# Optimization experiments

Measured on AMD Instinct MI355X. Metric: run time of the kernel, lower is better.

Reference implementation:

```python
import jax, jax.numpy as jnp
import numpy as np
import math

D_MODEL, N_HEADS, D_FF = 512, 8, 2048
B, S = 4, 2048
EPS = 1e-6


def _layernorm(x, alpha, bias):
    # Faithful to the torch module: std is unbiased (ddof=1) and eps is added to std, not var.
    m = jnp.mean(x, axis=-1, keepdims=True)
    s = jnp.std(x, axis=-1, keepdims=True, ddof=1)
    return alpha * (x - m) / (s + EPS) + bias


def setup_inputs() -> dict:
    key = jax.random.key(0)
    ks = jax.random.split(key, 16)
    d, f = D_MODEL, D_FF
    sd = 1.0 / math.sqrt(d)
    sf = 1.0 / math.sqrt(f)
    return {
        "x": jax.random.normal(ks[0], (B, S, d), jnp.float32),
        "wq": jax.random.normal(ks[1], (d, d), jnp.float32) * sd,
        "bq": jnp.zeros((d,), jnp.float32),
        "wk": jax.random.normal(ks[2], (d, d), jnp.float32) * sd,
        "bk": jnp.zeros((d,), jnp.float32),
        "wv": jax.random.normal(ks[3], (d, d), jnp.float32) * sd,
        "bv": jnp.zeros((d,), jnp.float32),
        "wo": jax.random.normal(ks[4], (d, d), jnp.float32) * sd,
        "bo": jnp.zeros((d,), jnp.float32),
        "w1": jax.random.normal(ks[5], (d, f), jnp.float32) * sd,
        "b1": jnp.zeros((f,), jnp.float32),
        "w2": jax.random.normal(ks[6], (f, d), jnp.float32) * sf,
        "b2": jnp.zeros((d,), jnp.float32),
        "ln1_a": jnp.ones((d,), jnp.float32),
        "ln1_b": jnp.zeros((d,), jnp.float32),
        "ln2_a": jnp.ones((d,), jnp.float32),
        "ln2_b": jnp.zeros((d,), jnp.float32),
    }


def reference(x, wq, bq, wk, bk, wv, bv, wo, bo, w1, b1, w2, b2, ln1_a, ln1_b, ln2_a, ln2_b):
    b, s, d = x.shape
    h, dk = N_HEADS, d // N_HEADS
    # QKV projections -> [b, h, s, dk]
    q = (x @ wq + bq).reshape(b, s, h, dk).transpose(0, 2, 1, 3)
    k = (x @ wk + bk).reshape(b, s, h, dk).transpose(0, 2, 1, 3)
    v = (x @ wv + bv).reshape(b, s, h, dk).transpose(0, 2, 1, 3)
    # Manual scaled-dot-product attention (no mask in EncoderBlock path)
    scores = jnp.einsum("bhqd,bhkd->bhqk", q, k) / jnp.sqrt(jnp.float32(dk))
    probs = jax.nn.softmax(scores, axis=-1)
    attn = jnp.einsum("bhqk,bhkd->bhqd", probs, v)
    concat = attn.transpose(0, 2, 1, 3).reshape(b, s, d)
    mha_out = concat @ wo + bo
    # Residual + LayerNorm 1
    y = _layernorm(x + mha_out, ln1_a, ln1_b)
    # FFN + Residual + LayerNorm 2
    ff = jax.nn.relu(y @ w1 + b1) @ w2 + b2
    return _layernorm(y + ff, ln2_a, ln2_b)
```

## Files before the change

### kernel.cpp

```cpp
#include <hip/hip_runtime.h>
#include <hip/hip_bf16.h>


typedef __bf16 bf16;
typedef __bf16 bf16x4 __attribute__((ext_vector_type(4)));
typedef __bf16 bf16x8 __attribute__((ext_vector_type(8)));
typedef float  f32x4  __attribute__((ext_vector_type(4)));

#define NBATCH 4
#define SEQ    2048
#define DMODEL 512
#define NHEADS 8
#define DHEAD  64
#define DFF    2048
#define MTOT   (NBATCH * SEQ)
#define WS_NEED 73416704u
#define QSCALE (0.125f * 1.44269504f)

__device__ __forceinline__ f32x4 mfma16(bf16x8 a, bf16x8 b, f32x4 c) {
    return __builtin_amdgcn_mfma_f32_16x16x32_bf16(a, b, c, 0, 0, 0);
}

__device__ __forceinline__ void lds16(const bf16* g, bf16* l) {
    __builtin_amdgcn_global_load_lds(
        (const __attribute__((address_space(1))) void*)g,
        (__attribute__((address_space(3))) void*)l, 16, 0, 0);
}

__device__ __forceinline__ float scrub(float f) {
    return (fabsf(f) < 1e30f) ? f : 0.f;
}

__device__ __forceinline__ void xcd_swizzle(int BMv, int BNv, int& mb, int& nb) {
    int gx = gridDim.x, gy = gridDim.y;
    int lin = blockIdx.y * gx + blockIdx.x;
    int q = (gx * gy) >> 3;
    lin = (lin & 7) * q + (lin >> 3);
    int mbi = lin / gy, nbi = lin - mbi * gy;
    mb = mbi * BMv; nb = nbi * BNv;
}

__global__ void sentinel_kernel(bf16* out) {
    out[threadIdx.x] = (bf16)1000.0f;
}

__global__ __launch_bounds__(256) void prep_kernel(
        const float* x,
        const float* wq, const float* wk, const float* wv, const float* wo,
        const float* w1, const float* w2,
        const float* bq, const float* bk, const float* bv, const float* bo,
        const float* b1, const float* b2,
        const float* l1a, const float* l1b, const float* l2a, const float* l2b,
        bf16* __restrict__ xcv,
        bf16* __restrict__ wT, bf16* __restrict__ w1T, bf16* __restrict__ w2T,
        bf16* __restrict__ prm) {
    __shared__ bf16 tile[32][33];
    int b = blockIdx.x;
    if (b < 4096) {
        int i = (b * 256 + threadIdx.x) * 4;
        float4 f = *(const float4*)(x + i);
        bf16x4 o = {(bf16)scrub(f.x), (bf16)scrub(f.y),
                    (bf16)scrub(f.z), (bf16)scrub(f.w)};
        *(bf16x4*)(xcv + i) = o;
        return;
    }
    if (b < 4106) {
        int pb = b - 4096;
        const float* srcs[10] = {bq, bk, bv, bo, b1, b2, l1a, l1b, l2a, l2b};
        const int len[10] = {512,512,512,512,2048,512,512,512,512,512};
        const int dst[10] = {0,512,1024,1536,2048,4096,4608,5120,5632,6144};
        const float* s = srcs[pb];
        bf16* d = prm + dst[pb];
        for (int i = threadIdx.x; i < len[pb]; i += 256)
            d[i] = (bf16)scrub(s[i]);
        return;
    }
    const float* in; bf16* out; int K, N, bx, by;
    if (b < 5130) {
        int idx = b - 4106, z = idx >> 8, rem = idx & 255;
        const float* srcs[4] = {wq, wk, wv, wo};
        in = srcs[z]; out = wT + (size_t)z * 262144;
        K = 512; N = 512; bx = rem & 15; by = rem >> 4;
    } else if (b < 6154) {
        int idx = b - 5130;
        in = w1; out = w1T; K = 512; N = 2048; bx = idx & 63; by = idx >> 6;
    } else {
        int idx = b - 6154;
        in = w2; out = w2T; K = 2048; N = 512; bx = idx & 15; by = idx >> 4;
    }
    int tx = threadIdx.x & 31, ty = threadIdx.x >> 5;
    int n0 = bx * 32, k0 = by * 32;
#pragma unroll
    for (int i = 0; i < 4; i++) {
        int kl = ty * 4 + i;
        tile[kl][tx] = (bf16)scrub(in[(size_t)(k0 + kl) * N + n0 + tx]);
    }
    __syncthreads();
#pragma unroll
    for (int i = 0; i < 4; i++) {
        int nl = ty * 4 + i;
        out[(size_t)(n0 + nl) * K + k0 + tx] = tile[tx][nl];
    }
}

template <bool RELU>
__global__ __launch_bounds__(256) void gemm_bt(
        const bf16* __restrict__ A, const bf16* __restrict__ BT,
        const bf16* __restrict__ bias, bf16* __restrict__ Cout,
        int M, int N, int K) {
    constexpr int BM = 128, BN = 128;
    __shared__ __align__(16) bf16 As0[BM * 32], As1[BM * 32];
    __shared__ __align__(16) bf16 Bs0[BN * 32], Bs1[BN * 32];

    int tid  = threadIdx.x;
    int wid  = tid >> 6, lane = tid & 63;
    int quad = lane >> 4, l15 = lane & 15;
    int mb, nb;
    xcd_swizzle(BM, BN, mb, nb);
    int wm = (wid >> 1) * 64, wn = (wid & 1) * 64;

    f32x4 acc[4][4] = {};

    int c0 = wid * 128 + lane, c1 = c0 + 64;
    int ar0 = c0 >> 2, ac0 = (c0 & 3) * 8;
    int ar1 = c1 >> 2, ac1 = (c1 & 3) * 8;
    int o0 = wid * 1024, o1 = wid * 1024 + 512;

    for (int k0 = 0; k0 < K; k0 += 64) {
        __syncthreads();
        lds16(&A [(size_t)(mb + ar0) * K + k0 + ac0],      &As0[o0]);
        lds16(&A [(size_t)(mb + ar1) * K + k0 + ac1],      &As0[o1]);
        lds16(&A [(size_t)(mb + ar0) * K + k0 + 32 + ac0], &As1[o0]);
        lds16(&A [(size_t)(mb + ar1) * K + k0 + 32 + ac1], &As1[o1]);
        lds16(&BT[(size_t)(nb + ar0) * K + k0 + ac0],      &Bs0[o0]);
        lds16(&BT[(size_t)(nb + ar1) * K + k0 + ac1],      &Bs0[o1]);
        lds16(&BT[(size_t)(nb + ar0) * K + k0 + 32 + ac0], &Bs1[o0]);
        lds16(&BT[(size_t)(nb + ar1) * K + k0 + 32 + ac1], &Bs1[o1]);
        __syncthreads();

        bf16x8 af[4], bfr[4];
#pragma unroll
        for (int i = 0; i < 4; i++)
            af[i] = *(const bf16x8*)&As0[(wm + i * 16 + l15) * 32 + quad * 8];
#pragma unroll
        for (int j = 0; j < 4; j++)
            bfr[j] = *(const bf16x8*)&Bs0[(wn + j * 16 + l15) * 32 + quad * 8];
#pragma unroll
        for (int i = 0; i < 4; i++)
#pragma unroll
            for (int j = 0; j < 4; j++)
                acc[i][j] = mfma16(af[i], bfr[j], acc[i][j]);
#pragma unroll
        for (int i = 0; i < 4; i++)
            af[i] = *(const bf16x8*)&As1[(wm + i * 16 + l15) * 32 + quad * 8];
#pragma unroll
        for (int j = 0; j < 4; j++)
            bfr[j] = *(const bf16x8*)&Bs1[(wn + j * 16 + l15) * 32 + quad * 8];
#pragma unroll
        for (int i = 0; i < 4; i++)
#pragma unroll
            for (int j = 0; j < 4; j++)
                acc[i][j] = mfma16(af[i], bfr[j], acc[i][j]);
    }

#pragma unroll
    for (int j = 0; j < 4; j++) {
        int n = nb + wn + j * 16 + l15;
        float bv = (float)bias[n];
#pragma unroll
        for (int i = 0; i < 4; i++) {
            int mBase = mb + wm + i * 16 + quad * 4;
#pragma unroll
            for (int r = 0; r < 4; r++) {
                float v = acc[i][j][r] + bv;
                if (RELU) v = v > 0.f ? v : 0.f;
                Cout[(size_t)(mBase + r) * N + n] = (bf16)v;
            }
        }
    }
}

template <bool RELU>
__global__ __launch_bounds__(256) void gemm_bt64(
        const bf16* __restrict__ A, const bf16* __restrict__ BT,
        const bf16* __restrict__ bias, bf16* __restrict__ Cout,
        int M, int N, int K) {
    constexpr int BM = 64, BN = 128;
    __shared__ __align__(16) bf16 As0[BM * 32], As1[BM * 32];
    __shared__ __align__(16) bf16 Bs0[BN * 32], Bs1[BN * 32];

    int tid  = threadIdx.x;
    int wid  = tid >> 6, lane = tid & 63;
    int quad = lane >> 4, l15 = lane & 15;
    int mb, nb;
    xcd_swizzle(BM, BN, mb, nb);
    int wm = (wid >> 1) * 32, wn = (wid & 1) * 64;

    f32x4 acc[2][4] = {};

    int cA = wid * 64 + lane;
    int arA = cA >> 2, acA = (cA & 3) * 8;
    int cB0 = wid * 128 + lane, cB1 = cB0 + 64;
    int br0 = cB0 >> 2, bc0 = (cB0 & 3) * 8;
    int br1 = cB1 >> 2, bc1 = (cB1 & 3) * 8;

    for (int k0 = 0; k0 < K; k0 += 64) {
        __syncthreads();
        lds16(&A [(size_t)(mb + arA) * K + k0 + acA],      &As0[wid * 512]);
        lds16(&A [(size_t)(mb + arA) * K + k0 + 32 + acA], &As1[wid * 512]);
        lds16(&BT[(size_t)(nb + br0) * K + k0 + bc0],      &Bs0[wid * 1024]);
        lds16(&BT[(size_t)(nb + br1) * K + k0 + bc1],      &Bs0[wid * 1024 + 512]);
        lds16(&BT[(size_t)(nb + br0) * K + k0 + 32 + bc0], &Bs1[wid * 1024]);
        lds16(&BT[(size_t)(nb + br1) * K + k0 + 32 + bc1], &Bs1[wid * 1024 + 512]);
        __syncthreads();

        bf16x8 a0[2], a1[2], b0[4], b1[4];
#pragma unroll
        for (int i = 0; i < 2; i++) {
            a0[i] = *(const bf16x8*)&As0[(wm + i * 16 + l15) * 32 + quad * 8];
            a1[i] = *(const bf16x8*)&As1[(wm + i * 16 + l15) * 32 + quad * 8];
        }
#pragma unroll
        for (int j = 0; j < 4; j++) {
            b0[j] = *(const bf16x8*)&Bs0[(wn + j * 16 + l15) * 32 + quad * 8];
            b1[j] = *(const bf16x8*)&Bs1[(wn + j * 16 + l15) * 32 + quad * 8];
        }
#pragma unroll
        for (int i = 0; i < 2; i++)
#pragma unroll
            for (int j = 0; j < 4; j++)
                acc[i][j] = mfma16(a1[i], b1[j], mfma16(a0[i], b0[j], acc[i][j]));
    }

#pragma unroll
    for (int j = 0; j < 4; j++) {
        int n = nb + wn + j * 16 + l15;
        float bv = (float)bias[n];
#pragma unroll
        for (int i = 0; i < 2; i++) {
            int mBase = mb + wm + i * 16 + quad * 4;
#pragma unroll
            for (int r = 0; r < 4; r++) {
                float v = acc[i][j][r] + bv;
                if (RELU) v = v > 0.f ? v : 0.f;
                Cout[(size_t)(mBase + r) * N + n] = (bf16)v;
            }
        }
    }
}

__global__ __launch_bounds__(256) void gemm_qkv(
        const bf16* __restrict__ A, const bf16* __restrict__ BT,
        const bf16* __restrict__ bias,
        bf16* __restrict__ Cq, bf16* __restrict__ Ck, bf16* __restrict__ Cv,
        int M, int N, int K) {
    constexpr int BM = 128, BN = 128;
    __shared__ __align__(16) bf16 As0[BM * 32], As1[BM * 32];
    __shared__ __align__(16) bf16 Bs0[BN * 32], Bs1[BN * 32];
    __shared__ __align__(16) bf16 Ts[128 * 136];

    int tid  = threadIdx.x;
    int wid  = tid >> 6, lane = tid & 63;
    int quad = lane >> 4, l15 = lane & 15;
    int mb, nb;
    xcd_swizzle(BM, BN, mb, nb);
    int wm = (wid >> 1) * 64, wn = (wid & 1) * 64;

    f32x4 acc[4][4] = {};

    int c0 = wid * 128 + lane, c1 = c0 + 64;
    int ar0 = c0 >> 2, ac0 = (c0 & 3) * 8;
    int ar1 = c1 >> 2, ac1 = (c1 & 3) * 8;
    int o0 = wid * 1024, o1 = wid * 1024 + 512;

    for (int k0 = 0; k0 < K; k0 += 64) {
        __syncthreads();
        lds16(&A [(size_t)(mb + ar0) * K + k0 + ac0],      &As0[o0]);
        lds16(&A [(size_t)(mb + ar1) * K + k0 + ac1],      &As0[o1]);
        lds16(&A [(size_t)(mb + ar0) * K + k0 + 32 + ac0], &As1[o0]);
        lds16(&A [(size_t)(mb + ar1) * K + k0 + 32 + ac1], &As1[o1]);
        lds16(&BT[(size_t)(nb + ar0) * K + k0 + ac0],      &Bs0[o0]);
        lds16(&BT[(size_t)(nb + ar1) * K + k0 + ac1],      &Bs0[o1]);
        lds16(&BT[(size_t)(nb + ar0) * K + k0 + 32 + ac0], &Bs1[o0]);
        lds16(&BT[(size_t)(nb + ar1) * K + k0 + 32 + ac1], &Bs1[o1]);
        __syncthreads();

        bf16x8 af[4], bfr[4];
#pragma unroll
        for (int i = 0; i < 4; i++)
            af[i] = *(const bf16x8*)&As0[(wm + i * 16 + l15) * 32 + quad * 8];
#pragma unroll
        for (int j = 0; j < 4; j++)
            bfr[j] = *(const bf16x8*)&Bs0[(wn + j * 16 + l15) * 32 + quad * 8];
#pragma unroll
        for (int i = 0; i < 4; i++)
#pragma unroll
            for (int j = 0; j < 4; j++)
                acc[i][j] = mfma16(af[i], bfr[j], acc[i][j]);
#pragma unroll
        for (int i = 0; i < 4; i++)
            af[i] = *(const bf16x8*)&As1[(wm + i * 16 + l15) * 32 + quad * 8];
#pragma unroll
        for (int j = 0; j < 4; j++)
            bfr[j] = *(const bf16x8*)&Bs1[(wn + j * 16 + l15) * 32 + quad * 8];
#pragma unroll
        for (int i = 0; i < 4; i++)
#pragma unroll
            for (int j = 0; j < 4; j++)
                acc[i][j] = mfma16(af[i], bfr[j], acc[i][j]);
    }

    int reg = nb >> 9;
    if (reg < 2) {
        bf16* C = reg ? Ck : Cq;
        float scl = reg ? 1.0f : QSCALE;
#pragma unroll
        for (int j = 0; j < 4; j++) {
            int n = nb + wn + j * 16 + l15;
            float bv = (float)bias[n];
            int nn = n & 511;
            int h = nn >> 6, dk = nn & 63;
#pragma unroll
            for (int i = 0; i < 4; i++) {
                int mBase = mb + wm + i * 16 + quad * 4;
#pragma unroll
                for (int r = 0; r < 4; r++) {
                    float v = (acc[i][j][r] + bv) * scl;
                    int m = mBase + r;
                    int b = m >> 11, s = m & (SEQ - 1);
                    C[((size_t)(b * NHEADS + h) * SEQ + s) * DHEAD + dk] = (bf16)v;
                }
            }
        }
    } else {
#pragma unroll
        for (int j = 0; j < 4; j++) {
            int nl = wn + j * 16 + l15;
            float bv = (float)bias[nb + nl];
#pragma unroll
            for (int i = 0; i < 4; i++) {
                int ml = wm + i * 16 + quad * 4;
                bf16x4 pk;
#pragma unroll
                for (int r = 0; r < 4; r++) pk[r] = (bf16)(acc[i][j][r] + bv);
                *(bf16x4*)&Ts[nl * 136 + ml] = pk;
            }
        }
        __syncthreads();
        int nl = tid >> 1, half = tid & 1;
        int nn = (nb + nl) & 511;
        int h = nn >> 6, dk = nn & 63;
        int bb = mb >> 11, s0 = mb & (SEQ - 1);
        bf16* dst = &Cv[((size_t)(bb * NHEADS + h) * DHEAD + dk) * SEQ + s0 + half * 64];
        const bf16* srcl = &Ts[nl * 136 + half * 64];
#pragma unroll
        for (int v = 0; v < 8; v++)
            *(uint4*)(dst + v * 8) = *(const uint4*)(srcl + v * 8);
    }
}

__global__ __launch_bounds__(256) void attn_kernel(
        const bf16* __restrict__ Q, const bf16* __restrict__ K,
        const bf16* __restrict__ VT, bf16* __restrict__ Out) {
    __shared__ __align__(16) bf16 Ks[2][64 * 72];
    __shared__ __align__(16) bf16 Vs[2][64 * 72];
    __shared__ __align__(16) bf16 Pb[4][16 * 80];
    int tid  = threadIdx.x;
    int wid  = tid >> 6, lane = tid & 63;
    int quad = lane >> 4, l15 = lane & 15;

    int lin = blockIdx.y * 16 + blockIdx.x;
    lin = (lin & 7) * 64 + (lin >> 3);
    int bh = lin >> 4;
    int qb = (lin & 15) * 128 + wid * 32;

    const bf16* Qh = Q  + (size_t)bh * SEQ * DHEAD;
    const bf16* Kh = K  + (size_t)bh * SEQ * DHEAD;
    const bf16* Vh = VT + (size_t)bh * DHEAD * SEQ;

    bf16x8 bQ0[2], bQ1[2];
#pragma unroll
    for (int c = 0; c < 2; c++) {
        const bf16* qp = &Qh[(qb + c * 16 + l15) * DHEAD + quad * 8];
        bQ0[c] = *(const bf16x8*)qp;
        bQ1[c] = *(const bf16x8*)(qp + 32);
    }

    bf16x8 vONE;
#pragma unroll
    for (int i = 0; i < 8; i++) vONE[i] = (bf16)1.0f;

    int cc0 = tid * 2, cc1 = cc0 + 1;
    int kr0 = cc0 >> 3, kc0 = (cc0 & 7) * 8;
    int kr1 = cc1 >> 3, kc1 = (cc1 & 7) * 8;

    f32x4 lacc[2] = {};
    f32x4 Oacc[2][4] = {};

    {
        uint4 ka0 = *(const uint4*)&Kh[(size_t)kr0 * DHEAD + kc0];
        uint4 ka1 = *(const uint4*)&Kh[(size_t)kr1 * DHEAD + kc1];
        uint4 va0 = *(const uint4*)&Vh[(size_t)kr0 * SEQ + kc0];
        uint4 va1 = *(const uint4*)&Vh[(size_t)kr1 * SEQ + kc1];
        *(uint4*)&Ks[0][kr0 * 72 + kc0] = ka0;
        *(uint4*)&Ks[0][kr1 * 72 + kc1] = ka1;
        *(uint4*)&Vs[0][kr0 * 72 + kc0] = va0;
        *(uint4*)&Vs[0][kr1 * 72 + kc1] = va1;
    }
    __syncthreads();

    for (int it = 0; it < SEQ / 64; it++) {
        int cur = it & 1, nxt = cur ^ 1;
        int kb = (it + 1) * 64;
        uint4 nk0, nk1, nv0, nv1;
        bool pf = (it + 1 < SEQ / 64);
        if (pf) {
            nk0 = *(const uint4*)&Kh[(size_t)(kb + kr0) * DHEAD + kc0];
            nk1 = *(const uint4*)&Kh[(size_t)(kb + kr1) * DHEAD + kc1];
            nv0 = *(const uint4*)&Vh[(size_t)kr0 * SEQ + kb + kc0];
            nv1 = *(const uint4*)&Vh[(size_t)kr1 * SEQ + kb + kc1];
        }

        bf16x8 aK0[4], aK1[4], bV0[4], bV1[4];
#pragma unroll
        for (int t = 0; t < 4; t++) {
            const bf16* kp = &Ks[cur][(t * 16 + l15) * 72 + quad * 8];
            aK0[t] = *(const bf16x8*)kp;
            aK1[t] = *(const bf16x8*)(kp + 32);
            const bf16* vp = &Vs[cur][(t * 16 + l15) * 72 + quad * 8];
            bV0[t] = *(const bf16x8*)vp;
            bV1[t] = *(const bf16x8*)(vp + 32);
        }

#pragma unroll
        for (int c = 0; c < 2; c++) {
            __builtin_amdgcn_s_setprio(1);
            f32x4 st[4];
#pragma unroll
            for (int t = 0; t < 4; t++) {
                f32x4 zv = {0.f, 0.f, 0.f, 0.f};
                st[t] = mfma16(aK1[t], bQ1[c], mfma16(aK0[t], bQ0[c], zv));
            }
            bf16* myP = Pb[wid];
#pragma unroll
            for (int t = 0; t < 4; t++) {
                bf16x4 pk;
#pragma unroll
                for (int r = 0; r < 4; r++)
                    pk[r] = (bf16)__builtin_amdgcn_exp2f(fminf(st[t][r], 60.f));
                *(bf16x4*)&myP[l15 * 80 + t * 16 + quad * 4] = pk;
            }
            bf16x8 aP0 = *(const bf16x8*)&myP[l15 * 80 + quad * 8];
            bf16x8 aP1 = *(const bf16x8*)&myP[l15 * 80 + 32 + quad * 8];
#pragma unroll
            for (int nt = 0; nt < 4; nt++)
                Oacc[c][nt] = mfma16(aP1, bV1[nt],
                                     mfma16(aP0, bV0[nt], Oacc[c][nt]));
            lacc[c] = mfma16(aP1, vONE, mfma16(aP0, vONE, lacc[c]));
            __builtin_amdgcn_s_setprio(0);
        }

        if (pf) {
            *(uint4*)&Ks[nxt][kr0 * 72 + kc0] = nk0;
            *(uint4*)&Ks[nxt][kr1 * 72 + kc1] = nk1;
            *(uint4*)&Vs[nxt][kr0 * 72 + kc0] = nv0;
            *(uint4*)&Vs[nxt][kr1 * 72 + kc1] = nv1;
        }
        __syncthreads();
    }

    int b = bh >> 3, hd = bh & 7;
#pragma unroll
    for (int c = 0; c < 2; c++) {
        float linv[4];
#pragma unroll
        for (int r = 0; r < 4; r++)
            linv[r] = 1.f / lacc[c][r];
#pragma unroll
        for (int nt = 0; nt < 4; nt++)
#pragma unroll
            for (int r = 0; r < 4; r++) {
                int s = qb + c * 16 + quad * 4 + r;
                Out[((size_t)(b * SEQ + s)) * DMODEL + hd * 64 + nt * 16 + l15]
                    = (bf16)(Oacc[c][nt][r] * linv[r]);
            }
    }
}

__global__ __launch_bounds__(256) void ln_kernel(
        const bf16* __restrict__ X, const bf16* __restrict__ T,
        const bf16* __restrict__ Al, const bf16* __restrict__ Bl,
        void* __restrict__ Out, int final_out) {
    int wid = threadIdx.x >> 6, lane = threadIdx.x & 63;
    int row = blockIdx.x * 4 + wid;
    const bf16* xr = X + (size_t)row * DMODEL;
    const bf16* tr = T + (size_t)row * DMODEL;
    bf16x8 xv = *(const bf16x8*)&xr[lane * 8];
    bf16x8 tv = *(const bf16x8*)&tr[lane * 8];
    float v[8];
#pragma unroll
    for (int i = 0; i < 8; i++) v[i] = (float)xv[i] + (float)tv[i];
    float sum = 0.f, sq = 0.f;
#pragma unroll
    for (int i = 0; i < 8; i++) { sum += v[i]; sq += v[i] * v[i]; }
#pragma unroll
    for (int m = 1; m < 64; m <<= 1) {
        sum += __shfl_xor(sum, m);
        sq  += __shfl_xor(sq,  m);
    }
    float mean = sum * (1.f / DMODEL);
    float var  = (sq - DMODEL * mean * mean) * (1.f / (DMODEL - 1));
    var = var > 0.f ? var : 0.f;
    float inv = 1.f / (sqrtf(var) + 1e-6f);
#pragma unroll
    for (int i = 0; i < 8; i++) {
        int c = lane * 8 + i;
        float yv = (float)Al[c] * (v[i] - mean) * inv + (float)Bl[c];
        yv = fminf(fmaxf(yv, -1e4f), 1e4f);
        size_t idx = (size_t)row * DMODEL + c;
        if (final_out) ((float*)Out)[idx] = yv;
        else           ((bf16*)Out)[idx]  = (bf16)yv;
    }
}

extern "C" void kernel_launch(void* const* d_in, const int* in_sizes, int n_in,
                              void* d_out, int out_size, void* d_ws, size_t ws_size,
                              hipStream_t stream) {
    if (ws_size < WS_NEED) {
        sentinel_kernel<<<1, 64, 0, stream>>>((bf16*)d_out);
        return;
    }

    const float* x  = (const float*)d_in[0];
    const float* wq = (const float*)d_in[1],  *bq = (const float*)d_in[2];
    const float* wk = (const float*)d_in[3],  *bk = (const float*)d_in[4];
    const float* wv = (const float*)d_in[5],  *bv = (const float*)d_in[6];
    const float* wo = (const float*)d_in[7],  *bo = (const float*)d_in[8];
    const float* w1 = (const float*)d_in[9],  *b1 = (const float*)d_in[10];
    const float* w2 = (const float*)d_in[11], *b2 = (const float*)d_in[12];
    const float* ln1a = (const float*)d_in[13], *ln1b = (const float*)d_in[14];
    const float* ln2a = (const float*)d_in[15], *ln2b = (const float*)d_in[16];

    char* ws = (char*)d_ws;
    bf16* wT   = (bf16*)(ws + 0);
    bf16* woT  = (bf16*)(ws + 1572864);
    bf16* w1T  = (bf16*)(ws + 2097152);
    bf16* w2T  = (bf16*)(ws + 4194304);
    bf16* xcv  = (bf16*)(ws + 6291456);
    bf16* prm  = (bf16*)(ws + 14680064);
    bf16* regA = (bf16*)(ws + 14696448);
    bf16* regB = (bf16*)(ws + 23085056);
    bf16* regC = (bf16*)(ws + 31473664);
    bf16* ff1  = (bf16*)(ws + 39862272);
    bf16* aout = (bf16*)d_out;

    bf16 *pbq = prm, *pbo = prm + 1536;
    bf16 *pb1 = prm + 2048, *pb2 = prm + 4096;
    bf16 *pl1a = prm + 4608, *pl1b = prm + 5120;
    bf16 *pl2a = prm + 5632, *pl2b = prm + 6144;

    prep_kernel<<<7178, 256, 0, stream>>>(x, wq, wk, wv, wo, w1, w2,
                                          bq, bk, bv, bo, b1, b2,
                                          ln1a, ln1b, ln2a, ln2b,
                                          xcv, wT, w1T, w2T, prm);

    gemm_qkv<<<dim3(64, 12), 256, 0, stream>>>(xcv, wT, pbq,
                                               regA, regB, regC,
                                               MTOT, 3 * DMODEL, DMODEL);

    attn_kernel<<<dim3(SEQ / 128, NBATCH * NHEADS), 256, 0, stream>>>(
        regA, regB, regC, aout);

    gemm_bt64<false><<<dim3(128, 4), 256, 0, stream>>>(aout, woT, pbo, regA,
                                                       MTOT, DMODEL, DMODEL);

    ln_kernel<<<MTOT / 4, 256, 0, stream>>>(xcv, regA, pl1a, pl1b, regB, 0);

    gemm_bt<true ><<<dim3(64, 16), 256, 0, stream>>>(regB, w1T, pb1, ff1,
                                                     MTOT, DFF, DMODEL);
    gemm_bt64<false><<<dim3(128, 4), 256, 0, stream>>>(ff1, w2T, pb2, regA,
                                                       MTOT, DMODEL, DFF);

    ln_kernel<<<MTOT / 4, 256, 0, stream>>>(regB, regA, pl2a, pl2b, d_out, 1);
}
```

Before: 283.4 us.

## Split attention over key halves and merge partials in a combine kernel

Splits each attention query block's key range into two halves processed by separate workgroups, doubling the grid to raise occupancy and parallelism. Each half writes unnormalized fp32 partial outputs and row sums, and a new combine kernel adds them and normalizes into bf16. This works without max-tracking because softmax here uses no max subtraction. The cost is extra fp32 traffic (two 16MB partial buffers plus sums) and another kernel launch. It also shrinks the P scratch stride from 80 to 72.

```diff
diff --git a/kernel.cpp b/kernel.cpp
--- a/kernel.cpp
+++ b/kernel.cpp
@@ -361,18 +361,23 @@
 
 __global__ __launch_bounds__(256) void attn_kernel(
         const bf16* __restrict__ Q, const bf16* __restrict__ K,
-        const bf16* __restrict__ VT, bf16* __restrict__ Out) {
+        const bf16* __restrict__ VT,
+        float* __restrict__ O1f, float* __restrict__ O2f,
+        float* __restrict__ L1, float* __restrict__ L2) {
     __shared__ __align__(16) bf16 Ks[2][64 * 72];
     __shared__ __align__(16) bf16 Vs[2][64 * 72];
-    __shared__ __align__(16) bf16 Pb[4][16 * 80];
+    __shared__ __align__(16) bf16 Pb[4][16 * 72];
     int tid  = threadIdx.x;
     int wid  = tid >> 6, lane = tid & 63;
     int quad = lane >> 4, l15 = lane & 15;
 
     int lin = blockIdx.y * 16 + blockIdx.x;
-    lin = (lin & 7) * 64 + (lin >> 3);
-    int bh = lin >> 4;
-    int qb = (lin & 15) * 128 + wid * 32;
+    lin = (lin & 7) * 128 + (lin >> 3);
+    int bh    = lin >> 5;
+    int rem   = lin & 31;
+    int qb    = ((rem >> 1) & 15) * 128 + wid * 32;
+    int split = rem & 1;
+    int kbase = split * (SEQ / 2);
 
     const bf16* Qh = Q  + (size_t)bh * SEQ * DHEAD;
     const bf16* Kh = K  + (size_t)bh * SEQ * DHEAD;
@@ -398,10 +403,10 @@
     f32x4 Oacc[2][4] = {};
 
     {
-        uint4 ka0 = *(const uint4*)&Kh[(size_t)kr0 * DHEAD + kc0];
-        uint4 ka1 = *(const uint4*)&Kh[(size_t)kr1 * DHEAD + kc1];
-        uint4 va0 = *(const uint4*)&Vh[(size_t)kr0 * SEQ + kc0];
-        uint4 va1 = *(const uint4*)&Vh[(size_t)kr1 * SEQ + kc1];
+        uint4 ka0 = *(const uint4*)&Kh[(size_t)(kbase + kr0) * DHEAD + kc0];
+        uint4 ka1 = *(const uint4*)&Kh[(size_t)(kbase + kr1) * DHEAD + kc1];
+        uint4 va0 = *(const uint4*)&Vh[(size_t)kr0 * SEQ + kbase + kc0];
+        uint4 va1 = *(const uint4*)&Vh[(size_t)kr1 * SEQ + kbase + kc1];
         *(uint4*)&Ks[0][kr0 * 72 + kc0] = ka0;
         *(uint4*)&Ks[0][kr1 * 72 + kc1] = ka1;
         *(uint4*)&Vs[0][kr0 * 72 + kc0] = va0;
@@ -409,11 +414,11 @@
     }
     __syncthreads();
 
-    for (int it = 0; it < SEQ / 64; it++) {
+    for (int it = 0; it < SEQ / 128; it++) {
         int cur = it & 1, nxt = cur ^ 1;
-        int kb = (it + 1) * 64;
+        int kb = kbase + (it + 1) * 64;
         uint4 nk0, nk1, nv0, nv1;
-        bool pf = (it + 1 < SEQ / 64);
+        bool pf = (it + 1 < SEQ / 128);
         if (pf) {
             nk0 = *(const uint4*)&Kh[(size_t)(kb + kr0) * DHEAD + kc0];
             nk1 = *(const uint4*)&Kh[(size_t)(kb + kr1) * DHEAD + kc1];
@@ -448,10 +453,10 @@
 #pragma unroll
                 for (int r = 0; r < 4; r++)
                     pk[r] = (bf16)__builtin_amdgcn_exp2f(fminf(st[t][r], 60.f));
-                *(bf16x4*)&myP[l15 * 80 + t * 16 + quad * 4] = pk;
-            }
-            bf16x8 aP0 = *(const bf16x8*)&myP[l15 * 80 + quad * 8];
-            bf16x8 aP1 = *(const bf16x8*)&myP[l15 * 80 + 32 + quad * 8];
+                *(bf16x4*)&myP[l15 * 72 + t * 16 + quad * 4] = pk;
+            }
+            bf16x8 aP0 = *(const bf16x8*)&myP[l15 * 72 + quad * 8];
+            bf16x8 aP1 = *(const bf16x8*)&myP[l15 * 72 + 32 + quad * 8];
 #pragma unroll
             for (int nt = 0; nt < 4; nt++)
                 Oacc[c][nt] = mfma16(aP1, bV1[nt],
@@ -469,22 +474,44 @@
         __syncthreads();
     }
 
+    float* Op = split ? O2f : O1f;
+    float* lp = split ? L2  : L1;
     int b = bh >> 3, hd = bh & 7;
 #pragma unroll
     for (int c = 0; c < 2; c++) {
-        float linv[4];
-#pragma unroll
-        for (int r = 0; r < 4; r++)
-            linv[r] = 1.f / lacc[c][r];
 #pragma unroll
         for (int nt = 0; nt < 4; nt++)
 #pragma unroll
             for (int r = 0; r < 4; r++) {
                 int s = qb + c * 16 + quad * 4 + r;
-                Out[((size_t)(b * SEQ + s)) * DMODEL + hd * 64 + nt * 16 + l15]
-                    = (bf16)(Oacc[c][nt][r] * linv[r]);
-            }
-    }
+                Op[((size_t)(b * SEQ + s)) * DMODEL + hd * 64 + nt * 16 + l15]
+                    = Oacc[c][nt][r];
+            }
+        if (l15 == 0) {
+#pragma unroll
+            for (int r = 0; r < 4; r++) {
+                int s = qb + c * 16 + quad * 4 + r;
+                lp[(size_t)(b * SEQ + s) * NHEADS + hd] = lacc[c][r];
+            }
+        }
+    }
+}
+
+__global__ __launch_bounds__(256) void combine_kernel(
+        const float* __restrict__ O1, const float* __restrict__ O2,
+        const float* __restrict__ L1, const float* __restrict__ L2,
+        bf16* __restrict__ Out) {
+    int e = blockIdx.x * 256 + threadIdx.x;
+    int row = e >> 7;
+    int hd  = ((e & 127) * 4) >> 6;
+    float l1 = L1[(size_t)row * NHEADS + hd];
+    float l2 = L2[(size_t)row * NHEADS + hd];
+    float inv = 1.f / (l1 + l2);
+    float4 a = ((const float4*)O1)[e];
+    float4 b = ((const float4*)O2)[e];
+    bf16x4 o = {(bf16)((a.x + b.x) * inv), (bf16)((a.y + b.y) * inv),
+                (bf16)((a.z + b.z) * inv), (bf16)((a.w + b.w) * inv)};
+    *(bf16x4*)(Out + (size_t)e * 4) = o;
 }
 
 __global__ __launch_bounds__(256) void ln_kernel(
@@ -552,7 +579,11 @@
     bf16* regB = (bf16*)(ws + 23085056);
     bf16* regC = (bf16*)(ws + 31473664);
     bf16* ff1  = (bf16*)(ws + 39862272);
-    bf16* aout = (bf16*)d_out;
+    float* O1f   = (float*)(ws + 39862272);
+    float* Lp1   = (float*)(ws + 39862272 + 16777216);
+    float* Lp2   = (float*)(ws + 39862272 + 17039360);
+    bf16*  aout2 = (bf16*) (ws + 39862272 + 17301504);
+    float* O2f   = (float*)d_out;
 
     bf16 *pbq = prm, *pbo = prm + 1536;
     bf16 *pb1 = prm + 2048, *pb2 = prm + 4096;
@@ -568,10 +599,12 @@
                                                regA, regB, regC,
                                                MTOT, 3 * DMODEL, DMODEL);
 
-    attn_kernel<<<dim3(SEQ / 128, NBATCH * NHEADS), 256, 0, stream>>>(
-        regA, regB, regC, aout);
-
-    gemm_bt64<false><<<dim3(128, 4), 256, 0, stream>>>(aout, woT, pbo, regA,
+    attn_kernel<<<dim3(16, 64), 256, 0, stream>>>(
+        regA, regB, regC, O1f, O2f, Lp1, Lp2);
+
+    combine_kernel<<<4096, 256, 0, stream>>>(O1f, O2f, Lp1, Lp2, aout2);
+
+    gemm_bt64<false><<<dim3(128, 4), 256, 0, stream>>>(aout2, woT, pbo, regA,
                                                        MTOT, DMODEL, DMODEL);
 
     ln_kernel<<<MTOT / 4, 256, 0, stream>>>(xcv, regA, pl1a, pl1b, regB, 0);
```

Result: slower. 291.4 us (+2.8%).

## Software-pipeline GEMM K-halves across buffers and repad attention P buffer

Applied to the files above, without the earlier changes.

The three GEMM kernels now issue the global-to-LDS load of the next K-step's first half while the current second half is being computed, instead of loading both halves and then computing. The aim is to hide global load latency behind MFMA work. Each iteration still has two barriers, and the ping-pong scheme depends on correct ordering between the halves. The attention kernel's per-wave P staging buffer row stride changes from 80 to 72 elements, which changes LDS bank mapping and shrinks the buffer.

```diff
diff --git a/kernel.cpp b/kernel.cpp
--- a/kernel.cpp
+++ b/kernel.cpp
@@ -126,41 +126,53 @@
     int ar1 = c1 >> 2, ac1 = (c1 & 3) * 8;
     int o0 = wid * 1024, o1 = wid * 1024 + 512;
 
+    lds16(&A [(size_t)(mb + ar0) * K + ac0], &As0[o0]);
+    lds16(&A [(size_t)(mb + ar1) * K + ac1], &As0[o1]);
+    lds16(&BT[(size_t)(nb + ar0) * K + ac0], &Bs0[o0]);
+    lds16(&BT[(size_t)(nb + ar1) * K + ac1], &Bs0[o1]);
+    __syncthreads();
+
     for (int k0 = 0; k0 < K; k0 += 64) {
-        __syncthreads();
-        lds16(&A [(size_t)(mb + ar0) * K + k0 + ac0],      &As0[o0]);
-        lds16(&A [(size_t)(mb + ar1) * K + k0 + ac1],      &As0[o1]);
         lds16(&A [(size_t)(mb + ar0) * K + k0 + 32 + ac0], &As1[o0]);
         lds16(&A [(size_t)(mb + ar1) * K + k0 + 32 + ac1], &As1[o1]);
-        lds16(&BT[(size_t)(nb + ar0) * K + k0 + ac0],      &Bs0[o0]);
-        lds16(&BT[(size_t)(nb + ar1) * K + k0 + ac1],      &Bs0[o1]);
         lds16(&BT[(size_t)(nb + ar0) * K + k0 + 32 + ac0], &Bs1[o0]);
         lds16(&BT[(size_t)(nb + ar1) * K + k0 + 32 + ac1], &Bs1[o1]);
-        __syncthreads();
-
-        bf16x8 af[4], bfr[4];
-#pragma unroll
-        for (int i = 0; i < 4; i++)
-            af[i] = *(const bf16x8*)&As0[(wm + i * 16 + l15) * 32 + quad * 8];
-#pragma unroll
-        for (int j = 0; j < 4; j++)
-            bfr[j] = *(const bf16x8*)&Bs0[(wn + j * 16 + l15) * 32 + quad * 8];
-#pragma unroll
-        for (int i = 0; i < 4; i++)
+        {
+            bf16x8 af[4], bfr[4];
+#pragma unroll
+            for (int i = 0; i < 4; i++)
+                af[i] = *(const bf16x8*)&As0[(wm + i * 16 + l15) * 32 + quad * 8];
 #pragma unroll
             for (int j = 0; j < 4; j++)
-                acc[i][j] = mfma16(af[i], bfr[j], acc[i][j]);
-#pragma unroll
-        for (int i = 0; i < 4; i++)
-            af[i] = *(const bf16x8*)&As1[(wm + i * 16 + l15) * 32 + quad * 8];
-#pragma unroll
-        for (int j = 0; j < 4; j++)
-            bfr[j] = *(const bf16x8*)&Bs1[(wn + j * 16 + l15) * 32 + quad * 8];
-#pragma unroll
-        for (int i = 0; i < 4; i++)
+                bfr[j] = *(const bf16x8*)&Bs0[(wn + j * 16 + l15) * 32 + quad * 8];
+#pragma unroll
+            for (int i = 0; i < 4; i++)
+#pragma unroll
+                for (int j = 0; j < 4; j++)
+                    acc[i][j] = mfma16(af[i], bfr[j], acc[i][j]);
+        }
+        __syncthreads();
+        if (k0 + 64 < K) {
+            lds16(&A [(size_t)(mb + ar0) * K + k0 + 64 + ac0], &As0[o0]);
+            lds16(&A [(size_t)(mb + ar1) * K + k0 + 64 + ac1], &As0[o1]);
+            lds16(&BT[(size_t)(nb + ar0) * K + k0 + 64 + ac0], &Bs0[o0]);
+            lds16(&BT[(size_t)(nb + ar1) * K + k0 + 64 + ac1], &Bs0[o1]);
+        }
+        {
+            bf16x8 af[4], bfr[4];
+#pragma unroll
+            for (int i = 0; i < 4; i++)
+                af[i] = *(const bf16x8*)&As1[(wm + i * 16 + l15) * 32 + quad * 8];
 #pragma unroll
             for (int j = 0; j < 4; j++)
-                acc[i][j] = mfma16(af[i], bfr[j], acc[i][j]);
+                bfr[j] = *(const bf16x8*)&Bs1[(wn + j * 16 + l15) * 32 + quad * 8];
+#pragma unroll
+            for (int i = 0; i < 4; i++)
+#pragma unroll
+                for (int j = 0; j < 4; j++)
+                    acc[i][j] = mfma16(af[i], bfr[j], acc[i][j]);
+        }
+        __syncthreads();
     }
 
 #pragma unroll
@@ -204,32 +216,50 @@
     int br0 = cB0 >> 2, bc0 = (cB0 & 3) * 8;
     int br1 = cB1 >> 2, bc1 = (cB1 & 3) * 8;
 
+    lds16(&A [(size_t)(mb + arA) * K + acA], &As0[wid * 512]);
+    lds16(&BT[(size_t)(nb + br0) * K + bc0], &Bs0[wid * 1024]);
+    lds16(&BT[(size_t)(nb + br1) * K + bc1], &Bs0[wid * 1024 + 512]);
+    __syncthreads();
+
     for (int k0 = 0; k0 < K; k0 += 64) {
-        __syncthreads();
-        lds16(&A [(size_t)(mb + arA) * K + k0 + acA],      &As0[wid * 512]);
         lds16(&A [(size_t)(mb + arA) * K + k0 + 32 + acA], &As1[wid * 512]);
-        lds16(&BT[(size_t)(nb + br0) * K + k0 + bc0],      &Bs0[wid * 1024]);
-        lds16(&BT[(size_t)(nb + br1) * K + k0 + bc1],      &Bs0[wid * 1024 + 512]);
         lds16(&BT[(size_t)(nb + br0) * K + k0 + 32 + bc0], &Bs1[wid * 1024]);
         lds16(&BT[(size_t)(nb + br1) * K + k0 + 32 + bc1], &Bs1[wid * 1024 + 512]);
-        __syncthreads();
-
-        bf16x8 a0[2], a1[2], b0[4], b1[4];
-#pragma unroll
-        for (int i = 0; i < 2; i++) {
-            a0[i] = *(const bf16x8*)&As0[(wm + i * 16 + l15) * 32 + quad * 8];
-            a1[i] = *(const bf16x8*)&As1[(wm + i * 16 + l15) * 32 + quad * 8];
-        }
-#pragma unroll
-        for (int j = 0; j < 4; j++) {
-            b0[j] = *(const bf16x8*)&Bs0[(wn + j * 16 + l15) * 32 + quad * 8];
-            b1[j] = *(const bf16x8*)&Bs1[(wn + j * 16 + l15) * 32 + quad * 8];
-        }
-#pragma unroll
-        for (int i = 0; i < 2; i++)
+        {
+            bf16x8 a0[2], b0[4];
+#pragma unroll
+            for (int i = 0; i < 2; i++)
+                a0[i] = *(const bf16x8*)&As0[(wm + i * 16 + l15) * 32 + quad * 8];
 #pragma unroll
             for (int j = 0; j < 4; j++)
-                acc[i][j] = mfma16(a1[i], b1[j], mfma16(a0[i], b0[j], acc[i][j]));
+                b0[j] = *(const bf16x8*)&Bs0[(wn + j * 16 + l15) * 32 + quad * 8];
+#pragma unroll
+            for (int i = 0; i < 2; i++)
+#pragma unroll
+                for (int j = 0; j < 4; j++)
+                    acc[i][j] = mfma16(a0[i], b0[j], acc[i][j]);
+        }
+        __syncthreads();
+        if (k0 + 64 < K) {
+            lds16(&A [(size_t)(mb + arA) * K + k0 + 64 + acA], &As0[wid * 512]);
+            lds16(&BT[(size_t)(nb + br0) * K + k0 + 64 + bc0], &Bs0[wid * 1024]);
+            lds16(&BT[(size_t)(nb + br1) * K + k0 + 64 + bc1], &Bs0[wid * 1024 + 512]);
+        }
+        {
+            bf16x8 a1[2], b1[4];
+#pragma unroll
+            for (int i = 0; i < 2; i++)
+                a1[i] = *(const bf16x8*)&As1[(wm + i * 16 + l15) * 32 + quad * 8];
+#pragma unroll
+            for (int j = 0; j < 4; j++)
+                b1[j] = *(const bf16x8*)&Bs1[(wn + j * 16 + l15) * 32 + quad * 8];
+#pragma unroll
+            for (int i = 0; i < 2; i++)
+#pragma unroll
+                for (int j = 0; j < 4; j++)
+                    acc[i][j] = mfma16(a1[i], b1[j], acc[i][j]);
+        }
+        __syncthreads();
     }
 
 #pragma unroll
@@ -273,41 +303,53 @@
     int ar1 = c1 >> 2, ac1 = (c1 & 3) * 8;
     int o0 = wid * 1024, o1 = wid * 1024 + 512;
 
+    lds16(&A [(size_t)(mb + ar0) * K + ac0], &As0[o0]);
+    lds16(&A [(size_t)(mb + ar1) * K + ac1], &As0[o1]);
+    lds16(&BT[(size_t)(nb + ar0) * K + ac0], &Bs0[o0]);
+    lds16(&BT[(size_t)(nb + ar1) * K + ac1], &Bs0[o1]);
+    __syncthreads();
+
     for (int k0 = 0; k0 < K; k0 += 64) {
-        __syncthreads();
-        lds16(&A [(size_t)(mb + ar0) * K + k0 + ac0],      &As0[o0]);
-        lds16(&A [(size_t)(mb + ar1) * K + k0 + ac1],      &As0[o1]);
         lds16(&A [(size_t)(mb + ar0) * K + k0 + 32 + ac0], &As1[o0]);
         lds16(&A [(size_t)(mb + ar1) * K + k0 + 32 + ac1], &As1[o1]);
-        lds16(&BT[(size_t)(nb + ar0) * K + k0 + ac0],      &Bs0[o0]);
-        lds16(&BT[(size_t)(nb + ar1) * K + k0 + ac1],      &Bs0[o1]);
         lds16(&BT[(size_t)(nb + ar0) * K + k0 + 32 + ac0], &Bs1[o0]);
         lds16(&BT[(size_t)(nb + ar1) * K + k0 + 32 + ac1], &Bs1[o1]);
-        __syncthreads();
-
-        bf16x8 af[4], bfr[4];
-#pragma unroll
-        for (int i = 0; i < 4; i++)
-            af[i] = *(const bf16x8*)&As0[(wm + i * 16 + l15) * 32 + quad * 8];
-#pragma unroll
-        for (int j = 0; j < 4; j++)
-            bfr[j] = *(const bf16x8*)&Bs0[(wn + j * 16 + l15) * 32 + quad * 8];
-#pragma unroll
-        for (int i = 0; i < 4; i++)
+        {
+            bf16x8 af[4], bfr[4];
+#pragma unroll
+            for (int i = 0; i < 4; i++)
+                af[i] = *(const bf16x8*)&As0[(wm + i * 16 + l15) * 32 + quad * 8];
 #pragma unroll
             for (int j = 0; j < 4; j++)
-                acc[i][j] = mfma16(af[i], bfr[j], acc[i][j]);
-#pragma unroll
-        for (int i = 0; i < 4; i++)
-            af[i] = *(const bf16x8*)&As1[(wm + i * 16 + l15) * 32 + quad * 8];
-#pragma unroll
-        for (int j = 0; j < 4; j++)
-            bfr[j] = *(const bf16x8*)&Bs1[(wn + j * 16 + l15) * 32 + quad * 8];
-#pragma unroll
-        for (int i = 0; i < 4; i++)
+                bfr[j] = *(const bf16x8*)&Bs0[(wn + j * 16 + l15) * 32 + quad * 8];
+#pragma unroll
+            for (int i = 0; i < 4; i++)
+#pragma unroll
+                for (int j = 0; j < 4; j++)
+                    acc[i][j] = mfma16(af[i], bfr[j], acc[i][j]);
+        }
+        __syncthreads();
+        if (k0 + 64 < K) {
+            lds16(&A [(size_t)(mb + ar0) * K + k0 + 64 + ac0], &As0[o0]);
+            lds16(&A [(size_t)(mb + ar1) * K + k0 + 64 + ac1], &As0[o1]);
+            lds16(&BT[(size_t)(nb + ar0) * K + k0 + 64 + ac0], &Bs0[o0]);
+            lds16(&BT[(size_t)(nb + ar1) * K + k0 + 64 + ac1], &Bs0[o1]);
+        }
+        {
+            bf16x8 af[4], bfr[4];
+#pragma unroll
+            for (int i = 0; i < 4; i++)
+                af[i] = *(const bf16x8*)&As1[(wm + i * 16 + l15) * 32 + quad * 8];
 #pragma unroll
             for (int j = 0; j < 4; j++)
-                acc[i][j] = mfma16(af[i], bfr[j], acc[i][j]);
+                bfr[j] = *(const bf16x8*)&Bs1[(wn + j * 16 + l15) * 32 + quad * 8];
+#pragma unroll
+            for (int i = 0; i < 4; i++)
+#pragma unroll
+                for (int j = 0; j < 4; j++)
+                    acc[i][j] = mfma16(af[i], bfr[j], acc[i][j]);
+        }
+        __syncthreads();
     }
 
     int reg = nb >> 9;
@@ -364,7 +406,7 @@
         const bf16* __restrict__ VT, bf16* __restrict__ Out) {
     __shared__ __align__(16) bf16 Ks[2][64 * 72];
     __shared__ __align__(16) bf16 Vs[2][64 * 72];
-    __shared__ __align__(16) bf16 Pb[4][16 * 80];
+    __shared__ __align__(16) bf16 Pb[4][16 * 72];
     int tid  = threadIdx.x;
     int wid  = tid >> 6, lane = tid & 63;
     int quad = lane >> 4, l15 = lane & 15;
@@ -448,10 +490,10 @@
 #pragma unroll
                 for (int r = 0; r < 4; r++)
                     pk[r] = (bf16)__builtin_amdgcn_exp2f(fminf(st[t][r], 60.f));
-                *(bf16x4*)&myP[l15 * 80 + t * 16 + quad * 4] = pk;
+                *(bf16x4*)&myP[l15 * 72 + t * 16 + quad * 4] = pk;
             }
-            bf16x8 aP0 = *(const bf16x8*)&myP[l15 * 80 + quad * 8];
-            bf16x8 aP1 = *(const bf16x8*)&myP[l15 * 80 + 32 + quad * 8];
+            bf16x8 aP0 = *(const bf16x8*)&myP[l15 * 72 + quad * 8];
+            bf16x8 aP1 = *(const bf16x8*)&myP[l15 * 72 + 32 + quad * 8];
 #pragma unroll
             for (int nt = 0; nt < 4; nt++)
                 Oacc[c][nt] = mfma16(aP1, bV1[nt],
```

Result: no change. 284.7 us (+0.4%).
